# Performance work log

Measured on AMD Instinct MI355X. Metric: run time of the kernel, lower is better.

Reference implementation:

```python
import jax, jax.numpy as jnp
import numpy as np


def _bidir_linear_rnn(x, kernel, rec):
    """Bidirectional SimpleRNN(units=1, activation=None, use_bias=False).
    x: [B, T, 1]; kernel, rec: [1, 1]. Returns [B, T, 2] (concat fw/bw).
    Linear recurrence h_t = k*x_t + r*h_{t-1} computed as an associative scan.
    """
    k = kernel[0, 0]
    r = rec[0, 0]

    def scan_dir(xs):
        u = xs * k                       # [B, T, 1]
        a = jnp.full_like(u, r)          # decay per step (constant)

        def combine(c1, c2):
            a1, b1 = c1
            a2, b2 = c2
            return (a1 * a2, a2 * b1 + b2)

        _, h = jax.lax.associative_scan(combine, (a, u), axis=1)
        return h                         # [B, T, 1]

    fw = scan_dir(x)
    bw = jnp.flip(scan_dir(jnp.flip(x, axis=1)), axis=1)
    return jnp.concatenate([fw, bw], axis=-1)  # [B, T, 2]


def setup_inputs() -> dict:
    key = jax.random.key(0)
    B, T, D = 4096, 4096, 1
    x = jax.random.normal(key, (B, T, D), dtype=jnp.float32)
    kernel = jnp.ones((1, 1), dtype=jnp.float32)           # toy_kernel = 1.0
    rec = -0.5 * jnp.ones((1, 1), dtype=jnp.float32)       # toy_recurrent_kernel = -0.5
    return {"x": x, "kernel": kernel, "rec": rec}


def reference(x, kernel, rec):
    out_stateless = _bidir_linear_rnn(x, kernel, rec)
    # Stateful layer has identical weights and zero initial states on first call,
    # so its output equals the stateless output; diff is their difference.
    out_stateful = _bidir_linear_rnn(x, kernel, rec)
    diff = out_stateful - out_stateless
    return (out_stateless, diff)
```

## Files before the change

kernel.cpp:

```cpp
#include <hip/hip_runtime.h>


constexpr int T_LEN = 4096;
constexpr int SEG   = 16;
constexpr int NT    = 256;

__global__ __launch_bounds__(NT) void bidir_rnn(
    const float* __restrict__ x,
    const float* __restrict__ kp,
    const float* __restrict__ rp,
    float*       __restrict__ out,
    float*       __restrict__ diff)
{
    const int b   = blockIdx.x;
    const int tid = threadIdx.x;
    const float k = *kp;
    const float r = *rp;

    float pw[SEG + 1];
    pw[0] = 1.0f;
    #pragma unroll
    for (int i = 1; i <= SEG; ++i) pw[i] = pw[i - 1] * r;

    const size_t rowbase = (size_t)b * T_LEN;

    const float4* xin = (const float4*)(x + rowbase + (size_t)tid * SEG);
    float4 v0 = xin[0], v1 = xin[1], v2 = xin[2], v3 = xin[3];
    float u[SEG] = {v0.x, v0.y, v0.z, v0.w, v1.x, v1.y, v1.z, v1.w,
                    v2.x, v2.y, v2.z, v2.w, v3.x, v3.y, v3.z, v3.w};
    #pragma unroll
    for (int j = 0; j < SEG; ++j) u[j] *= k;

    float lf[SEG], lb[SEG];
    lf[0] = u[0];
    #pragma unroll
    for (int j = 1; j < SEG; ++j) lf[j] = fmaf(r, lf[j - 1], u[j]);
    lb[SEG - 1] = u[SEG - 1];
    #pragma unroll
    for (int j = SEG - 2; j >= 0; --j) lb[j] = fmaf(r, lb[j + 1], u[j]);

    __shared__ float sA[NT], sB[NT];

    sA[tid] = pw[SEG];
    sB[tid] = lf[SEG - 1];
    __syncthreads();
    #pragma unroll
    for (int off = 1; off < NT; off <<= 1) {
        float a_cur = sA[tid], b_cur = sB[tid];
        float a_pre = 0.0f, b_pre = 0.0f;
        if (tid >= off) { a_pre = sA[tid - off]; b_pre = sB[tid - off]; }
        __syncthreads();
        if (tid >= off) {
            sA[tid] = a_pre * a_cur;
            sB[tid] = fmaf(a_cur, b_pre, b_cur);
        }
        __syncthreads();
    }
    const float Hf = (tid == 0) ? 0.0f : sB[tid - 1];
    __syncthreads();

    const int rt = (NT - 1) - tid;
    sA[rt] = pw[SEG];
    sB[rt] = lb[0];
    __syncthreads();
    #pragma unroll
    for (int off = 1; off < NT; off <<= 1) {
        float a_cur = sA[tid], b_cur = sB[tid];
        float a_pre = 0.0f, b_pre = 0.0f;
        if (tid >= off) { a_pre = sA[tid - off]; b_pre = sB[tid - off]; }
        __syncthreads();
        if (tid >= off) {
            sA[tid] = a_pre * a_cur;
            sB[tid] = fmaf(a_cur, b_pre, b_cur);
        }
        __syncthreads();
    }
    const float Hb = (rt == 0) ? 0.0f : sB[rt - 1];

    float fw[SEG], bw[SEG];
    #pragma unroll
    for (int j = 0; j < SEG; ++j) {
        fw[j] = fmaf(pw[j + 1],   Hf, lf[j]);
        bw[j] = fmaf(pw[SEG - j], Hb, lb[j]);
    }

    float4* o = (float4*)(out + (rowbase + (size_t)tid * SEG) * 2);
    #pragma unroll
    for (int m = 0; m < 8; ++m) {
        o[m] = make_float4(fw[2 * m], bw[2 * m], fw[2 * m + 1], bw[2 * m + 1]);
    }

    float4* d = (float4*)(diff + rowbase * 2) + tid;
    const float4 z = make_float4(0.0f, 0.0f, 0.0f, 0.0f);
    #pragma unroll
    for (int m = 0; m < 8; ++m) d[m * NT] = z;
}

extern "C" void kernel_launch(void* const* d_in, const int* in_sizes, int n_in,
                              void* d_out, int out_size, void* d_ws, size_t ws_size,
                              hipStream_t stream) {
    const float* x  = (const float*)d_in[0];
    const float* kp = (const float*)d_in[1];
    const float* rp = (const float*)d_in[2];
    float* out = (float*)d_out;

    const int B = in_sizes[0] / T_LEN;
    float* diff = out + (size_t)B * T_LEN * 2;

    bidir_rnn<<<dim3(B), dim3(NT), 0, stream>>>(x, kp, rp, out, diff);
}
```

Baseline: 324.4 us.

## Replace LDS block scans with wavefront shuffle scans and stage output through LDS

Replaces the two 256-thread shared-memory Hillis-Steele scans, which each need many block barriers, with intra-wavefront shuffle scans in both directions plus a small cross-wave combine through shared memory. The output is also staged through a padded LDS buffer, so each global store instruction writes a contiguous, fully coalesced span instead of each thread writing its own 128-byte strip. This removes most __syncthreads calls and should improve write coalescing. The cost is about 36KB of LDS per block, which may lower occupancy.

```diff
diff --git a/kernel.cpp b/kernel.cpp
--- a/kernel.cpp
+++ b/kernel.cpp
@@ -1,9 +1,12 @@
 #include <hip/hip_runtime.h>
 
 
-constexpr int T_LEN = 4096;
-constexpr int SEG   = 16;
-constexpr int NT    = 256;
+constexpr int T_LEN  = 4096;
+constexpr int SEG    = 16;
+constexpr int NT     = 256;
+constexpr int NW     = NT / 64;
+constexpr int ROW_F4 = T_LEN * 2 / 4;
+constexpr int LDS_F4 = (ROW_F4 / 8) * 9;
 
 __global__ __launch_bounds__(NT) void bidir_rnn(
     const float* __restrict__ x,
@@ -12,8 +15,10 @@
     float*       __restrict__ out,
     float*       __restrict__ diff)
 {
-    const int b   = blockIdx.x;
-    const int tid = threadIdx.x;
+    const int b    = blockIdx.x;
+    const int tid  = threadIdx.x;
+    const int lane = tid & 63;
+    const int wv   = tid >> 6;
     const float k = *kp;
     const float r = *rp;
 
@@ -21,10 +26,11 @@
     pw[0] = 1.0f;
     #pragma unroll
     for (int i = 1; i <= SEG; ++i) pw[i] = pw[i - 1] * r;
+    const float a16 = pw[SEG];
 
     const size_t rowbase = (size_t)b * T_LEN;
 
-    const float4* xin = (const float4*)(x + rowbase + (size_t)tid * SEG);
+    const float4* xin = (const float4*)(x + rowbase) + tid * 4;
     float4 v0 = xin[0], v1 = xin[1], v2 = xin[2], v3 = xin[3];
     float u[SEG] = {v0.x, v0.y, v0.z, v0.w, v1.x, v1.y, v1.z, v1.w,
                     v2.x, v2.y, v2.z, v2.w, v3.x, v3.y, v3.z, v3.w};
@@ -39,55 +45,63 @@
     #pragma unroll
     for (int j = SEG - 2; j >= 0; --j) lb[j] = fmaf(r, lb[j + 1], u[j]);
 
-    __shared__ float sA[NT], sB[NT];
+    float af = a16, bf = lf[SEG - 1];
+    #pragma unroll
+    for (int off = 1; off < 64; off <<= 1) {
+        float ap = __shfl_up(af, off);
+        float bp = __shfl_up(bf, off);
+        if (lane >= off) { bf = fmaf(af, bp, bf); af *= ap; }
+    }
+    float aef = __shfl_up(af, 1), bef = __shfl_up(bf, 1);
+    if (lane == 0) { aef = 1.0f; bef = 0.0f; }
 
-    sA[tid] = pw[SEG];
-    sB[tid] = lf[SEG - 1];
-    __syncthreads();
+    float ab = a16, bb = lb[0];
     #pragma unroll
-    for (int off = 1; off < NT; off <<= 1) {
-        float a_cur = sA[tid], b_cur = sB[tid];
-        float a_pre = 0.0f, b_pre = 0.0f;
-        if (tid >= off) { a_pre = sA[tid - off]; b_pre = sB[tid - off]; }
-        __syncthreads();
-        if (tid >= off) {
-            sA[tid] = a_pre * a_cur;
-            sB[tid] = fmaf(a_cur, b_pre, b_cur);
-        }
-        __syncthreads();
+    for (int off = 1; off < 64; off <<= 1) {
+        float ap = __shfl_down(ab, off);
+        float bp = __shfl_down(bb, off);
+        if (lane < 64 - off) { bb = fmaf(ab, bp, bb); ab *= ap; }
     }
-    const float Hf = (tid == 0) ? 0.0f : sB[tid - 1];
+    float aeb = __shfl_down(ab, 1), beb = __shfl_down(bb, 1);
+    if (lane == 63) { aeb = 1.0f; beb = 0.0f; }
+
+    __shared__ float4 sOut[LDS_F4];
+    __shared__ float sWa[NW], sWb[NW], sVa[NW], sVb[NW];
+    if (lane == 63) { sWa[wv] = af; sWb[wv] = bf; }
+    if (lane == 0)  { sVa[wv] = ab; sVb[wv] = bb; }
     __syncthreads();
 
-    const int rt = (NT - 1) - tid;
-    sA[rt] = pw[SEG];
-    sB[rt] = lb[0];
+    float Pb = 0.0f;
+    #pragma unroll
+    for (int w = 0; w < NW - 1; ++w) {
+        if (w < wv) { Pb = fmaf(sWa[w], Pb, sWb[w]); }
+    }
+    const float Hf = fmaf(aef, Pb, bef);
+
+    float Qb = 0.0f;
+    #pragma unroll
+    for (int w = NW - 1; w > 0; --w) {
+        if (w > wv) { Qb = fmaf(sVa[w], Qb, sVb[w]); }
+    }
+    const float Hb = fmaf(aeb, Qb, beb);
+
+    #pragma unroll
+    for (int q = 0; q < 8; ++q) {
+        const int j0 = 2 * q, j1 = 2 * q + 1;
+        float4 o;
+        o.x = fmaf(pw[j0 + 1],   Hf, lf[j0]);
+        o.y = fmaf(pw[SEG - j0], Hb, lb[j0]);
+        o.z = fmaf(pw[j1 + 1],   Hf, lf[j1]);
+        o.w = fmaf(pw[SEG - j1], Hb, lb[j1]);
+        sOut[tid * 9 + q] = o;
+    }
     __syncthreads();
+
+    float4* orow = (float4*)(out + rowbase * 2);
     #pragma unroll
-    for (int off = 1; off < NT; off <<= 1) {
-        float a_cur = sA[tid], b_cur = sB[tid];
-        float a_pre = 0.0f, b_pre = 0.0f;
-        if (tid >= off) { a_pre = sA[tid - off]; b_pre = sB[tid - off]; }
-        __syncthreads();
-        if (tid >= off) {
-            sA[tid] = a_pre * a_cur;
-            sB[tid] = fmaf(a_cur, b_pre, b_cur);
-        }
-        __syncthreads();
-    }
-    const float Hb = (rt == 0) ? 0.0f : sB[rt - 1];
-
-    float fw[SEG], bw[SEG];
-    #pragma unroll
-    for (int j = 0; j < SEG; ++j) {
-        fw[j] = fmaf(pw[j + 1],   Hf, lf[j]);
-        bw[j] = fmaf(pw[SEG - j], Hb, lb[j]);
-    }
-
-    float4* o = (float4*)(out + (rowbase + (size_t)tid * SEG) * 2);
-    #pragma unroll
-    for (int m = 0; m < 8; ++m) {
-        o[m] = make_float4(fw[2 * m], bw[2 * m], fw[2 * m + 1], bw[2 * m + 1]);
+    for (int q2 = 0; q2 < 8; ++q2) {
+        const int f4 = q2 * NT + tid;
+        orow[f4] = sOut[(f4 >> 3) * 9 + (f4 & 7)];
     }
 
     float4* d = (float4*)(diff + rowbase * 2) + tid;
```

After: 319.0 us. About the same (-1.7%).
